# Performance work log

Measured on AMD Instinct MI355X. Metric: run time of the kernel, lower is better.

## Reference

```python
import jax, jax.numpy as jnp
from jax import lax
import numpy as np

B, N, NPOINT, NSAMPLE, C = 4, 8192, 2048, 32, 128
RADIUS = 0.2
H1, H2, OUT = 64, 128, 128  # mlp: (3+C)->H1->H2, sas: H2->OUT


def fps(xyz, npoint):
    # furthest point sampling: xyz (B,N,3) -> idx (B,npoint) int32
    b, n, _ = xyz.shape
    init_idx = jnp.zeros((b,), jnp.int32)

    def step(carry, _):
        dist, last = carry
        p = jnp.take_along_axis(xyz, last[:, None, None], axis=1)  # (B,1,3)
        d = jnp.sum((xyz - p) ** 2, axis=-1)                       # (B,N)
        dist = jnp.minimum(dist, d)
        nxt = jnp.argmax(dist, axis=-1).astype(jnp.int32)
        return (dist, nxt), nxt

    (_, _), rest = lax.scan(step, (jnp.full((b, n), 1e10, jnp.float32), init_idx),
                            None, length=npoint - 1)
    return jnp.concatenate([init_idx[None, :], rest], axis=0).T    # (B,npoint)


def ball_query(xyz, new_xyz, radius, nsample):
    # xyz (B,N,3), new_xyz (B,S,3) -> idx (B,S,nsample) int32
    n = xyz.shape[1]
    d2 = jnp.sum((new_xyz[:, :, None, :] - xyz[:, None, :, :]) ** 2, axis=-1)  # (B,S,N)
    ar = jnp.arange(n, dtype=jnp.int32)
    keys = jnp.where(d2 <= radius * radius, ar, n)  # valid -> own index, invalid -> N
    neg_vals, _ = lax.top_k(-keys, nsample)          # smallest nsample keys
    idx = -neg_vals
    first = idx[..., :1]
    return jnp.where(idx >= n, first, idx)           # pad invalid with first valid


def gather_points(pts, idx):
    # pts (B,N,D), idx (B,S,ns) -> (B,S,ns,D)
    b, s, ns = idx.shape
    flat = jnp.take_along_axis(pts, idx.reshape(b, s * ns, 1), axis=1)
    return flat.reshape(b, s, ns, -1)


def setup_inputs() -> dict:
    key = jax.random.key(0)
    ks = jax.random.split(key, 8)
    xyz = jax.random.uniform(ks[0], (B, N, 3), dtype=jnp.float32)
    features = jax.random.normal(ks[1], (B, C, N), dtype=jnp.float32)
    cin = C + 3
    W1 = jax.random.normal(ks[2], (H1, cin), dtype=jnp.float32) / np.sqrt(cin)
    b1 = jnp.zeros((H1,), jnp.float32)
    W2 = jax.random.normal(ks[3], (H2, H1), dtype=jnp.float32) / np.sqrt(H1)
    b2 = jnp.zeros((H2,), jnp.float32)
    Wsa = jax.random.normal(ks[4], (OUT, H2), dtype=jnp.float32) / np.sqrt(H2)
    bsa = jnp.zeros((OUT,), jnp.float32)
    return {"xyz": xyz, "features": features, "W1": W1, "b1": b1,
            "W2": W2, "b2": b2, "Wsa": Wsa, "bsa": bsa}


def reference(xyz, features, W1, b1, W2, b2, Wsa, bsa):
    center_idx = fps(xyz, NPOINT)                                   # (B,S)
    new_xyz = jnp.take_along_axis(xyz, center_idx[:, :, None], axis=1)  # (B,S,3)
    g_idx = ball_query(xyz, new_xyz, RADIUS, NSAMPLE)               # (B,S,ns)
    g_xyz = gather_points(xyz, g_idx) - new_xyz[:, :, None, :]      # (B,S,ns,3) relative coords
    g_feat = gather_points(features.transpose(0, 2, 1), g_idx)      # (B,S,ns,C)
    h = jnp.concatenate([g_xyz, g_feat], axis=-1)                   # (B,S,ns,3+C)
    h = jax.nn.relu(jnp.einsum('bsnc,oc->bsno', h, W1) + b1)        # shared 1x1-conv MLP
    h = jax.nn.relu(jnp.einsum('bsnc,oc->bsno', h, W2) + b2)
    pooled = jnp.max(h, axis=2)                                     # max over nsample -> (B,S,H2)
    out = jnp.einsum('bsc,oc->bso', pooled, Wsa) + bsa              # sas channel mixer
    return new_xyz, out.transpose(0, 2, 1)                          # (B,S,3), (B,OUT,S)
```

## Files before the change

kernel.cpp:

```cpp
#include <hip/hip_runtime.h>
#include <cstdint>
#include <cstddef>

#define NB 4
#define NN 8192
#define NPTS 2048
#define NSAMP 32
#define NC 128
#define CIN 131
#define NH1 64
#define NH2 128
#define NOUTC 128

__device__ __forceinline__ float d2_exact(float ax, float ay, float az,
                                          float bx, float by, float bz) {
  float dx = ax - bx, dy = ay - by, dz = az - bz;
  return __fadd_rn(__fadd_rn(__fmul_rn(dx, dx), __fmul_rn(dy, dy)),
                   __fmul_rn(dz, dz));
}

__global__ __launch_bounds__(1024, 1) void fps_kernel(
    const float* __restrict__ xyz, float* __restrict__ newxyz) {
  const int b = blockIdx.x;
  const int tid = threadIdx.x;
  const float* xb = xyz + (size_t)b * NN * 3;
  float x[8], y[8], z[8], dist[8];
#pragma unroll
  for (int k = 0; k < 8; ++k) {
    int j = tid + (k << 10);
    x[k] = xb[j * 3 + 0];
    y[k] = xb[j * 3 + 1];
    z[k] = xb[j * 3 + 2];
    dist[k] = 1e10f;
  }
  __shared__ float sP[3];
  __shared__ float wv[16];
  __shared__ int wi[16];
  if (tid == 0) {
    sP[0] = x[0]; sP[1] = y[0]; sP[2] = z[0];
    newxyz[(size_t)b * NPTS * 3 + 0] = x[0];
    newxyz[(size_t)b * NPTS * 3 + 1] = y[0];
    newxyz[(size_t)b * NPTS * 3 + 2] = z[0];
  }
  __syncthreads();
  const int lane = tid & 63;
  const int wid = tid >> 6;
  for (int t = 1; t < NPTS; ++t) {
    float px = sP[0], py = sP[1], pz = sP[2];
    float bv = -1.0f;
    int bi = 0;
#pragma unroll
    for (int k = 0; k < 8; ++k) {
      float d = d2_exact(x[k], y[k], z[k], px, py, pz);
      float nd = fminf(dist[k], d);
      dist[k] = nd;
      if (nd > bv) { bv = nd; bi = tid + (k << 10); }
    }
#pragma unroll
    for (int off = 1; off < 64; off <<= 1) {
      float ov = __shfl_xor(bv, off);
      int oi = __shfl_xor(bi, off);
      if (ov > bv || (ov == bv && oi < bi)) { bv = ov; bi = oi; }
    }
    if (lane == 0) { wv[wid] = bv; wi[wid] = bi; }
    __syncthreads();
    float v2 = (lane < 16) ? wv[lane] : -1.0f;
    int i2 = (lane < 16) ? wi[lane] : 0x7fffffff;
#pragma unroll
    for (int off = 1; off < 16; off <<= 1) {
      float ov = __shfl_xor(v2, off);
      int oi = __shfl_xor(i2, off);
      if (ov > v2 || (ov == v2 && oi < i2)) { v2 = ov; i2 = oi; }
    }
    int sel = __shfl(i2, 0);
    if (tid == (sel & 1023)) {
      int k = sel >> 10;
      sP[0] = x[k]; sP[1] = y[k]; sP[2] = z[k];
      size_t o = ((size_t)b * NPTS + t) * 3;
      newxyz[o + 0] = x[k]; newxyz[o + 1] = y[k]; newxyz[o + 2] = z[k];
    }
    __syncthreads();
  }
}

__global__ __launch_bounds__(256) void ballq_kernel(
    const float* __restrict__ xyz, const float* __restrict__ newxyz,
    int* __restrict__ bidx) {
  const int cid = blockIdx.x * 4 + (threadIdx.x >> 6);
  const int lane = threadIdx.x & 63;
  const int b = cid >> 11;
  const float* xb = xyz + (size_t)b * NN * 3;
  const float cx = newxyz[(size_t)cid * 3 + 0];
  const float cy = newxyz[(size_t)cid * 3 + 1];
  const float cz = newxyz[(size_t)cid * 3 + 2];
  int* ob = bidx + (size_t)cid * NSAMP;
  int total = 0;
  int first = -1;
  for (int c0 = 0; c0 < NN; c0 += 64) {
    int j = c0 + lane;
    float xx = xb[j * 3 + 0], yy = xb[j * 3 + 1], zz = xb[j * 3 + 2];
    float d2 = d2_exact(cx, cy, cz, xx, yy, zz);
    bool in = d2 <= 0.04f;
    unsigned long long m = __ballot(in);
    if (first < 0 && m) first = c0 + __builtin_ctzll(m);
    int pos = total + __popcll(m & ((1ull << lane) - 1ull));
    if (in && pos < NSAMP) ob[pos] = j;
    total += __popcll(m);
    if (total >= NSAMP) break;
  }
  if (total < NSAMP && lane < NSAMP - total) ob[total + lane] = first;
}

__global__ void tw_kernel(const float* __restrict__ W1, const float* __restrict__ W2,
                          const float* __restrict__ Wsa, float* __restrict__ w1t,
                          float* __restrict__ w2t, float* __restrict__ wsat) {
  int i = blockIdx.x * blockDim.x + threadIdx.x;
  if (i < CIN * NH1) w1t[i] = W1[(i % NH1) * CIN + (i / NH1)];
  if (i < NH1 * NH2) w2t[i] = W2[(i % NH2) * NH1 + (i / NH2)];
  if (i < NH2 * NOUTC) wsat[i] = Wsa[(i % NOUTC) * NH2 + (i / NOUTC)];
}

__global__ void tfeat_kernel(const float* __restrict__ feat, float* __restrict__ featT) {
  __shared__ float tile[32][33];
  const int b = blockIdx.z;
  const int n0 = blockIdx.x * 32, c0 = blockIdx.y * 32;
  const int tx = threadIdx.x, ty = threadIdx.y;
#pragma unroll
  for (int r = 0; r < 4; ++r)
    tile[ty + r * 8][tx] = feat[((size_t)b * NC + c0 + ty + r * 8) * NN + n0 + tx];
  __syncthreads();
#pragma unroll
  for (int r = 0; r < 4; ++r)
    featT[((size_t)b * NN + n0 + ty + r * 8) * NC + c0 + tx] = tile[tx][ty + r * 8];
}

#define HS 36
__global__ __launch_bounds__(256) void mlp_kernel(
    const float* __restrict__ xyz, const float* __restrict__ fsrc,
    const float* __restrict__ newxyz, const int* __restrict__ bidx,
    const float* __restrict__ w1t, const float* __restrict__ b1,
    const float* __restrict__ w2t, const float* __restrict__ b2,
    const float* __restrict__ wsat, const float* __restrict__ bsa,
    float* __restrict__ out1, int useT) {
  __shared__ float h[CIN * HS];
  __shared__ float h1[NH1 * HS];
  __shared__ float pl[256];
  __shared__ float pooled[NH2];
  __shared__ int sidx[NSAMP];
  __shared__ float sc[3];
  const int cid = blockIdx.x;
  const int b = cid >> 11;
  const int s = cid & 2047;
  const int tid = threadIdx.x;
  if (tid < NSAMP) sidx[tid] = bidx[(size_t)cid * NSAMP + tid];
  if (tid < 3) sc[tid] = newxyz[(size_t)cid * 3 + tid];
  __syncthreads();
  {
    const int ss = tid >> 3, q = tid & 7;
    const int j = sidx[ss];
    if (useT) {
      const float4* fr = (const float4*)(fsrc + ((size_t)b * NN + j) * NC + q * 16);
#pragma unroll
      for (int u = 0; u < 4; ++u) {
        float4 v = fr[u];
        int c = 3 + q * 16 + u * 4;
        h[(c + 0) * HS + ss] = v.x;
        h[(c + 1) * HS + ss] = v.y;
        h[(c + 2) * HS + ss] = v.z;
        h[(c + 3) * HS + ss] = v.w;
      }
    } else {
      for (int u = 0; u < 16; ++u) {
        int c = q * 16 + u;
        h[(3 + c) * HS + ss] = fsrc[((size_t)b * NC + c) * NN + j];
      }
    }
    if (q == 0) {
      const float* pr = xyz + ((size_t)b * NN + j) * 3;
      h[0 * HS + ss] = pr[0] - sc[0];
      h[1 * HS + ss] = pr[1] - sc[1];
      h[2 * HS + ss] = pr[2] - sc[2];
    }
  }
  __syncthreads();
  {
    const int o = tid & 63, sg = tid >> 6;
    float acc[8];
    const float bb = b1[o];
#pragma unroll
    for (int i = 0; i < 8; ++i) acc[i] = bb;
    const float4* hb = (const float4*)&h[sg * 8];
    for (int k = 0; k < CIN; ++k) {
      float w = w1t[k * NH1 + o];
      float4 a = hb[k * (HS / 4) + 0];
      float4 c = hb[k * (HS / 4) + 1];
      acc[0] = fmaf(w, a.x, acc[0]); acc[1] = fmaf(w, a.y, acc[1]);
      acc[2] = fmaf(w, a.z, acc[2]); acc[3] = fmaf(w, a.w, acc[3]);
      acc[4] = fmaf(w, c.x, acc[4]); acc[5] = fmaf(w, c.y, acc[5]);
      acc[6] = fmaf(w, c.z, acc[6]); acc[7] = fmaf(w, c.w, acc[7]);
    }
#pragma unroll
    for (int i = 0; i < 8; ++i) h1[o * HS + sg * 8 + i] = fmaxf(acc[i], 0.0f);
  }
  __syncthreads();
  {
    const int o = tid & 127, sg = tid >> 7;
    float acc[16];
    const float bb = b2[o];
#pragma unroll
    for (int i = 0; i < 16; ++i) acc[i] = bb;
    const float4* hb = (const float4*)&h1[sg * 16];
    for (int k = 0; k < NH1; ++k) {
      float w = w2t[k * NH2 + o];
#pragma unroll
      for (int u = 0; u < 4; ++u) {
        float4 a = hb[k * (HS / 4) + u];
        acc[u * 4 + 0] = fmaf(w, a.x, acc[u * 4 + 0]);
        acc[u * 4 + 1] = fmaf(w, a.y, acc[u * 4 + 1]);
        acc[u * 4 + 2] = fmaf(w, a.z, acc[u * 4 + 2]);
        acc[u * 4 + 3] = fmaf(w, a.w, acc[u * 4 + 3]);
      }
    }
    float pm = acc[0];
#pragma unroll
    for (int i = 1; i < 16; ++i) pm = fmaxf(pm, acc[i]);
    pl[sg * 128 + o] = pm;
  }
  __syncthreads();
  if (tid < NH2) pooled[tid] = fmaxf(fmaxf(pl[tid], pl[128 + tid]), 0.0f);
  __syncthreads();
  if (tid < NOUTC) {
    float acc = bsa[tid];
    for (int k = 0; k < NH2; ++k) acc = fmaf(pooled[k], wsat[k * NOUTC + tid], acc);
    out1[((size_t)b * NOUTC + tid) * NPTS + s] = acc;
  }
}

extern "C" void kernel_launch(void* const* d_in, const int* in_sizes, int n_in,
                              void* d_out, int out_size, void* d_ws, size_t ws_size,
                              hipStream_t stream) {
  const float* xyz = (const float*)d_in[0];
  const float* feat = (const float*)d_in[1];
  const float* W1 = (const float*)d_in[2];
  const float* b1 = (const float*)d_in[3];
  const float* W2 = (const float*)d_in[4];
  const float* b2 = (const float*)d_in[5];
  const float* Wsa = (const float*)d_in[6];
  const float* bsa = (const float*)d_in[7];
  float* out = (float*)d_out;
  float* newxyz = out;
  float* out1 = out + (size_t)NB * NPTS * 3;

  const size_t featT_f = (size_t)NB * NN * NC;
  const size_t small_f = (size_t)CIN * NH1 + NH1 * NH2 + NH2 * NOUTC +
                         (size_t)NB * NPTS * NSAMP;
  float* ws = (float*)d_ws;
  bool useT = ws_size >= (featT_f + small_f) * 4;
  float* featT = ws;
  float* w1t = ws + (useT ? featT_f : 0);
  float* w2t = w1t + CIN * NH1;
  float* wsat = w2t + NH1 * NH2;
  int* bidx = (int*)(wsat + NH2 * NOUTC);

  tw_kernel<<<64, 256, 0, stream>>>(W1, W2, Wsa, w1t, w2t, wsat);
  if (useT)
    tfeat_kernel<<<dim3(NN / 32, NC / 32, NB), dim3(32, 8), 0, stream>>>(feat, featT);
  fps_kernel<<<NB, 1024, 0, stream>>>(xyz, newxyz);
  ballq_kernel<<<NB * NPTS / 4, 256, 0, stream>>>(xyz, newxyz, bidx);
  mlp_kernel<<<NB * NPTS, 256, 0, stream>>>(xyz, useT ? featT : feat, newxyz, bidx,
                                            w1t, b1, w2t, b2, wsat, bsa, out1,
                                            (int)useT);
}
```

Measured before the change: 3.952 ms.

## Restructure FPS loop with one barrier, DPP reductions, and packed distance math

The furthest-point-sampling kernel now needs one __syncthreads per iteration instead of two. Double-buffered shared slots hold each wavefront's best value, index and coordinates, so every thread can read the next centroid without a second barrier. Within-wavefront argmax reductions use DPP moves in place of most shuffles, and distance math uses 2-wide float vectors to allow packed FP32 ops. The risks are DPP row semantics (the 0x141/0x140 row mirrors must still combine all 16 lanes correctly) and the requirement that parity buffering avoids races between iterations.

```diff
diff --git a/kernel.cpp b/kernel.cpp
--- a/kernel.cpp
+++ b/kernel.cpp
@@ -12,6 +12,8 @@
 #define NH2 128
 #define NOUTC 128
 
+typedef float v2f __attribute__((ext_vector_type(2)));
+
 __device__ __forceinline__ float d2_exact(float ax, float ay, float az,
                                           float bx, float by, float bz) {
   float dx = ax - bx, dy = ay - by, dz = az - bz;
@@ -19,67 +21,117 @@
                    __fmul_rn(dz, dz));
 }
 
+#if __has_builtin(__builtin_amdgcn_mov_dpp)
+template <int CTRL>
+__device__ __forceinline__ float dppf(float v) {
+  return __int_as_float(
+      __builtin_amdgcn_mov_dpp(__float_as_int(v), CTRL, 0xF, 0xF, true));
+}
+template <int CTRL>
+__device__ __forceinline__ int dppi(int v) {
+  return __builtin_amdgcn_mov_dpp(v, CTRL, 0xF, 0xF, true);
+}
+#else
+template <int CTRL>
+__device__ __forceinline__ float dppf(float v) {
+  const int m = (CTRL == 0xB1) ? 1 : (CTRL == 0x4E) ? 2 : (CTRL == 0x141) ? 7 : 15;
+  return __shfl_xor(v, m);
+}
+template <int CTRL>
+__device__ __forceinline__ int dppi(int v) {
+  const int m = (CTRL == 0xB1) ? 1 : (CTRL == 0x4E) ? 2 : (CTRL == 0x141) ? 7 : 15;
+  return __shfl_xor(v, m);
+}
+#endif
+
+__device__ __forceinline__ void red_pair(float& bv, int& bi, float ov, int oi) {
+  bool t = (ov > bv) || (ov == bv && oi < bi);
+  bv = t ? ov : bv;
+  bi = t ? oi : bi;
+}
+
 __global__ __launch_bounds__(1024, 1) void fps_kernel(
     const float* __restrict__ xyz, float* __restrict__ newxyz) {
+#pragma clang fp contract(off)
   const int b = blockIdx.x;
   const int tid = threadIdx.x;
-  const float* xb = xyz + (size_t)b * NN * 3;
-  float x[8], y[8], z[8], dist[8];
-#pragma unroll
-  for (int k = 0; k < 8; ++k) {
-    int j = tid + (k << 10);
-    x[k] = xb[j * 3 + 0];
-    y[k] = xb[j * 3 + 1];
-    z[k] = xb[j * 3 + 2];
-    dist[k] = 1e10f;
-  }
-  __shared__ float sP[3];
-  __shared__ float wv[16];
-  __shared__ int wi[16];
-  if (tid == 0) {
-    sP[0] = x[0]; sP[1] = y[0]; sP[2] = z[0];
-    newxyz[(size_t)b * NPTS * 3 + 0] = x[0];
-    newxyz[(size_t)b * NPTS * 3 + 1] = y[0];
-    newxyz[(size_t)b * NPTS * 3 + 2] = z[0];
-  }
-  __syncthreads();
   const int lane = tid & 63;
   const int wid = tid >> 6;
+  const float* xb = xyz + (size_t)b * NN * 3;
+
+  v2f x2[4], y2[4], z2[4], dd[4];
+#pragma unroll
+  for (int p = 0; p < 4; ++p) {
+    int j0 = tid + ((2 * p) << 10);
+    int j1 = tid + ((2 * p + 1) << 10);
+    x2[p].x = xb[j0 * 3 + 0]; x2[p].y = xb[j1 * 3 + 0];
+    y2[p].x = xb[j0 * 3 + 1]; y2[p].y = xb[j1 * 3 + 1];
+    z2[p].x = xb[j0 * 3 + 2]; z2[p].y = xb[j1 * 3 + 2];
+    dd[p].x = 1e10f; dd[p].y = 1e10f;
+  }
+
+  __shared__ float vbuf[2][16];
+  __shared__ int ibuf[2][16];
+  __shared__ float cbuf[2][16][3];
+
+  float cx = xb[0], cy = xb[1], cz = xb[2];
+  if (tid == 0) {
+    newxyz[(size_t)b * NPTS * 3 + 0] = cx;
+    newxyz[(size_t)b * NPTS * 3 + 1] = cy;
+    newxyz[(size_t)b * NPTS * 3 + 2] = cz;
+  }
+
   for (int t = 1; t < NPTS; ++t) {
-    float px = sP[0], py = sP[1], pz = sP[2];
+    const int par = t & 1;
+    v2f pxv = {cx, cx}, pyv = {cy, cy}, pzv = {cz, cz};
     float bv = -1.0f;
     int bi = 0;
-#pragma unroll
-    for (int k = 0; k < 8; ++k) {
-      float d = d2_exact(x[k], y[k], z[k], px, py, pz);
-      float nd = fminf(dist[k], d);
-      dist[k] = nd;
-      if (nd > bv) { bv = nd; bi = tid + (k << 10); }
-    }
-#pragma unroll
-    for (int off = 1; off < 64; off <<= 1) {
-      float ov = __shfl_xor(bv, off);
-      int oi = __shfl_xor(bi, off);
-      if (ov > bv || (ov == bv && oi < bi)) { bv = ov; bi = oi; }
-    }
-    if (lane == 0) { wv[wid] = bv; wi[wid] = bi; }
+    float bwx = 0.f, bwy = 0.f, bwz = 0.f;
+#pragma unroll
+    for (int p = 0; p < 4; ++p) {
+      v2f dx = x2[p] - pxv;
+      v2f dy = y2[p] - pyv;
+      v2f dz = z2[p] - pzv;
+      v2f s = dx * dx + dy * dy + dz * dz;
+      v2f nd;
+      nd.x = fminf(dd[p].x, s.x);
+      nd.y = fminf(dd[p].y, s.y);
+      dd[p] = nd;
+      {
+        bool c = nd.x > bv;
+        bv = c ? nd.x : bv; bi = c ? (tid + ((2 * p) << 10)) : bi;
+        bwx = c ? x2[p].x : bwx; bwy = c ? y2[p].x : bwy; bwz = c ? z2[p].x : bwz;
+      }
+      {
+        bool c = nd.y > bv;
+        bv = c ? nd.y : bv; bi = c ? (tid + ((2 * p + 1) << 10)) : bi;
+        bwx = c ? x2[p].y : bwx; bwy = c ? y2[p].y : bwy; bwz = c ? z2[p].y : bwz;
+      }
+    }
+    red_pair(bv, bi, dppf<0xB1>(bv), dppi<0xB1>(bi));
+    red_pair(bv, bi, dppf<0x4E>(bv), dppi<0x4E>(bi));
+    red_pair(bv, bi, dppf<0x141>(bv), dppi<0x141>(bi));
+    red_pair(bv, bi, dppf<0x140>(bv), dppi<0x140>(bi));
+    red_pair(bv, bi, __shfl_xor(bv, 16), __shfl_xor(bi, 16));
+    red_pair(bv, bi, __shfl_xor(bv, 32), __shfl_xor(bi, 32));
+    if (tid == (bi & 1023)) {
+      vbuf[par][wid] = bv;
+      ibuf[par][wid] = bi;
+      cbuf[par][wid][0] = bwx; cbuf[par][wid][1] = bwy; cbuf[par][wid][2] = bwz;
+    }
     __syncthreads();
-    float v2 = (lane < 16) ? wv[lane] : -1.0f;
-    int i2 = (lane < 16) ? wi[lane] : 0x7fffffff;
-#pragma unroll
-    for (int off = 1; off < 16; off <<= 1) {
-      float ov = __shfl_xor(v2, off);
-      int oi = __shfl_xor(i2, off);
-      if (ov > v2 || (ov == v2 && oi < i2)) { v2 = ov; i2 = oi; }
-    }
-    int sel = __shfl(i2, 0);
-    if (tid == (sel & 1023)) {
-      int k = sel >> 10;
-      sP[0] = x[k]; sP[1] = y[k]; sP[2] = z[k];
+    float v2w = vbuf[par][lane & 15];
+    int i2w = ibuf[par][lane & 15];
+    red_pair(v2w, i2w, dppf<0xB1>(v2w), dppi<0xB1>(i2w));
+    red_pair(v2w, i2w, dppf<0x4E>(v2w), dppi<0x4E>(i2w));
+    red_pair(v2w, i2w, dppf<0x141>(v2w), dppi<0x141>(i2w));
+    red_pair(v2w, i2w, dppf<0x140>(v2w), dppi<0x140>(i2w));
+    const int slot = (i2w & 1023) >> 6;
+    cx = cbuf[par][slot][0]; cy = cbuf[par][slot][1]; cz = cbuf[par][slot][2];
+    if (tid == (i2w & 1023)) {
       size_t o = ((size_t)b * NPTS + t) * 3;
-      newxyz[o + 0] = x[k]; newxyz[o + 1] = y[k]; newxyz[o + 2] = z[k];
-    }
-    __syncthreads();
+      newxyz[o + 0] = cx; newxyz[o + 1] = cy; newxyz[o + 2] = cz;
+    }
   }
 }
 
```

New measurement: 3.740 ms. 1.06x faster.
